# Optimization experiments

Measured on AMD Instinct MI355X. Metric: run time of the kernel, lower is better.

Reference implementation:

```python
import jax, jax.numpy as jnp
import numpy as np
import math

N, E = 100000, 1600000
IN_FEATS, H, Z_DIM, D, B_COEF = 128, 128, 32, 2, 0.2


def calc_thetas(d):
    # Bernstein-basis thetas, ascending coefficients (matches calculate_theta2)
    thetas = []
    for i in range(d + 1):
        p1 = np.zeros(i + 1); p1[i] = 0.5 ** i               # (x/2)^i
        p2 = np.array([math.comb(d - i, j) * (-0.5) ** j for j in range(d - i + 1)])  # (1-x/2)^(d-i)
        coeffs = np.convolve(p1, p2)                          # length d+1, ascending
        beta = math.gamma(i + 1) * math.gamma(d + 1 - i) / math.gamma(d + 2)
        thetas.append((coeffs / beta).tolist())
    return thetas

THETAS = calc_thetas(D)


def linear(x, w, b):
    return x @ w.T + b


def polyconv(theta, feat, src, dst, d_invsqrt, n):
    h = theta[0] * feat
    for k in range(1, len(theta)):
        tmp = feat * d_invsqrt                                # [N, F]
        agg = jax.ops.segment_sum(tmp[src], dst, num_segments=n)
        feat = feat - agg * d_invsqrt                         # (I - D^-1/2 A D^-1/2) feat
        h = h + theta[k] * feat
    return h


def enc_dec(x, w1, b1, w2, b2, src, dst, d_invsqrt, n):
    x = jax.nn.relu(linear(x, w1, b1))
    hs = jnp.concatenate([polyconv(t, x, src, dst, d_invsqrt, n) for t in THETAS], axis=-1)
    return linear(hs, w2, b2)


def setup_inputs() -> dict:
    key = jax.random.key(0)
    ks = jax.random.split(key, 16)
    nb = len(THETAS)
    return {
        "features": jax.random.normal(ks[0], (N, IN_FEATS), jnp.float32),
        "src": jax.random.randint(ks[1], (E,), 0, N, jnp.int32),
        "dst": jax.random.randint(ks[2], (E,), 0, N, jnp.int32),
        "enc_w1": jax.random.normal(ks[3], (H, IN_FEATS), jnp.float32) * 0.05,
        "enc_b1": jnp.zeros((H,), jnp.float32),
        "enc_w2": jax.random.normal(ks[4], (H, H * nb), jnp.float32) * 0.05,
        "enc_b2": jnp.zeros((H,), jnp.float32),
        "dec_w1": jax.random.normal(ks[5], (IN_FEATS, H), jnp.float32) * 0.05,
        "dec_b1": jnp.zeros((IN_FEATS,), jnp.float32),
        "dec_w2": jax.random.normal(ks[6], (IN_FEATS, IN_FEATS * nb), jnp.float32) * 0.05,
        "dec_b2": jnp.zeros((IN_FEATS,), jnp.float32),
        "rep_w": jax.random.normal(ks[7], (Z_DIM, H), jnp.float32) * 0.05,
        "rep_b": jnp.zeros((Z_DIM,), jnp.float32),
        "rec_w": jax.random.normal(ks[8], (H, Z_DIM), jnp.float32) * 0.05,
        "rec_b": jnp.zeros((H,), jnp.float32),
        "disc_w": jax.random.uniform(ks[9], (H, H), jnp.float32, -1.0 / math.sqrt(H), 1.0 / math.sqrt(H)),
    }


def reference(features, src, dst, enc_w1, enc_b1, enc_w2, enc_b2,
              dec_w1, dec_b1, dec_w2, dec_b2, rep_w, rep_b, rec_w, rec_b, disc_w):
    n = features.shape[0]
    degs = jax.ops.segment_sum(jnp.ones((src.shape[0],), jnp.float32), dst, num_segments=n)
    d_invsqrt = jnp.maximum(degs, 1.0) ** -0.5
    d_invsqrt = d_invsqrt[:, None]

    positive = enc_dec(features, enc_w1, enc_b1, enc_w2, enc_b2, src, dst, d_invsqrt, n)
    perm = jax.random.permutation(jax.random.key(7), n)
    negative = enc_dec(features[perm], enc_w1, enc_b1, enc_w2, enc_b2, src, dst, d_invsqrt, n)

    summary = jax.nn.sigmoid(positive.mean(axis=0))           # [H]
    pos_dis = positive @ (disc_w @ summary)                   # [N]
    neg_dis = negative @ (disc_w @ summary)
    # BCEWithLogits: target=1 -> softplus(-x); target=0 -> softplus(x)
    dgi_loss = jnp.mean(jax.nn.softplus(-pos_dis)) + jnp.mean(jax.nn.softplus(neg_dis))

    mu = linear(positive, rep_w, rep_b)
    log_var = mu
    eps = jax.random.normal(jax.random.key(11), mu.shape, mu.dtype)
    z = mu + eps * jnp.exp(log_var / 2)

    x_rec = enc_dec(linear(z, rec_w, rec_b), dec_w1, dec_b1, dec_w2, dec_b2, src, dst, d_invsqrt, n)
    reconst_loss = jnp.sum((x_rec - features) ** 2)
    kl_div = -0.5 * jnp.sum(1 + log_var - mu ** 2 - jnp.exp(log_var))
    vgae_loss = reconst_loss + kl_div

    ratio = jax.lax.stop_gradient(dgi_loss / vgae_loss)
    return B_COEF * dgi_loss / ratio + (1 - B_COEF) * vgae_loss
```

## Files before the change

kernel.cpp:

```cpp
#include <hip/hip_runtime.h>
#include <math.h>

#define NN   100000
#define EE   1600000
#define F    128
#define ZD   32
#define SCAN_B 256
#define PREP_BLOCKS 161
#define FC1_BLOCKS  1563
#define ENC_BLOCKS  1563
#define NBUCK 391
#define PART_CHUNK 2048
#define PART_BLOCKS 782


typedef float f32x4 __attribute__((ext_vector_type(4)));
typedef int   i32x4 __attribute__((ext_vector_type(4)));
typedef __bf16 bf16x8 __attribute__((ext_vector_type(8)));

__device__ __forceinline__ f32x4 mfma16(i32x4 a, i32x4 b, f32x4 c) {
    return __builtin_amdgcn_mfma_f32_16x16x32_bf16(
        __builtin_bit_cast(bf16x8, a), __builtin_bit_cast(bf16x8, b), c, 0, 0, 0);
}

__device__ __forceinline__ unsigned f2bf(float f) {
    unsigned u = __float_as_uint(f);
    return (u + 0x7fffu + ((u >> 16) & 1u)) >> 16;
}
__device__ __forceinline__ float bf2f(unsigned h) { return __uint_as_float(h << 16); }

__device__ __forceinline__ unsigned pcg_hash(unsigned v) {
    v = v * 747796405u + 2891336453u;
    unsigned w = ((v >> ((v >> 28u) + 4u)) ^ v) * 277803737u;
    return (w >> 22u) ^ w;
}

__device__ __forceinline__ float block_reduce_sum(float v) {
    #pragma unroll
    for (int o = 32; o > 0; o >>= 1) v += __shfl_down(v, o, 64);
    __shared__ float s[8];
    int lane = threadIdx.x & 63, w = threadIdx.x >> 6;
    if (lane == 0) s[w] = v;
    __syncthreads();
    float t = 0.f;
    if (threadIdx.x == 0) {
        int nw = (blockDim.x + 63) >> 6;
        for (int i = 0; i < nw; ++i) t += s[i];
    }
    return t;
}

__global__ __launch_bounds__(256) void prep_deg_kernel(
        const float* __restrict__ repw, const float* __restrict__ w2e,
        const float* __restrict__ b2e,  const float* __restrict__ repb,
        const float* __restrict__ w2d,
        const float* __restrict__ w1d,  const float* __restrict__ recw,
        const float* __restrict__ recb, const float* __restrict__ b1d,
        const float* __restrict__ w1e,
        unsigned short* __restrict__ Wcat,
        float* __restrict__ bmu,
        unsigned short* __restrict__ wd2_a,
        unsigned short* __restrict__ wd2_b,
        unsigned short* __restrict__ wd2_c,
        unsigned short* __restrict__ wrd,
        float* __restrict__ brd,
        unsigned short* __restrict__ w1bf,
        const int* __restrict__ dst, int* __restrict__ degs, int e) {
    int bid = blockIdx.x, tid = threadIdx.x;
    if (bid >= PREP_BLOCKS) {
        int i = (bid - PREP_BLOCKS) * 256 + tid;
        if (i < e) atomicAdd(&degs[dst[i]], 1);
        return;
    }
    if (bid < 16) {
        int idx = bid * 256 + tid;
        int i = idx >> 7, k = idx & 127;
        float m0 = 0.f, m1 = 0.f, m2 = 0.f;
        for (int h = 0; h < 128; ++h) {
            float r = repw[i * 128 + h];
            const float* wr = w2e + (size_t)h * 384 + k;
            m0 += r * wr[0];
            m1 += r * wr[128];
            m2 += r * wr[256];
        }
        Wcat[(size_t)i * 128 + k]        = (unsigned short)f2bf(3.f * m0);
        Wcat[(size_t)(32 + i) * 128 + k] = (unsigned short)f2bf(3.f * (m1 - m0));
        Wcat[(size_t)(64 + i) * 128 + k] = (unsigned short)f2bf(0.75f * m0 - 1.5f * m1 + 0.75f * m2);
    } else if (bid == 16) {
        if (tid < 32) {
            float s = repb[tid];
            for (int h = 0; h < 128; ++h) s += repw[tid * 128 + h] * b2e[h];
            bmu[tid] = s;
        }
    } else if (bid < 81) {
        int idx = (bid - 17) * 256 + tid;
        int j = idx >> 7, k = idx & 127;
        const float* wr = w2d + (size_t)j * 384 + k;
        float w0 = wr[0], w1 = wr[128], w2v = wr[256];
        wd2_a[idx] = (unsigned short)f2bf(3.f * w0);
        wd2_b[idx] = (unsigned short)f2bf(3.f * (w1 - w0));
        wd2_c[idx] = (unsigned short)f2bf(0.75f * w0 - 1.5f * w1 + 0.75f * w2v);
    } else if (bid < 97) {
        int idx = (bid - 81) * 256 + tid;
        int j = idx >> 5, i = idx & 31;
        float s = 0.f;
        for (int h = 0; h < 128; ++h) s += w1d[j * 128 + h] * recw[h * 32 + i];
        wrd[idx] = (unsigned short)f2bf(s);
        if (idx < 128) {
            float b = b1d[idx];
            for (int h = 0; h < 128; ++h) b += w1d[idx * 128 + h] * recb[h];
            brd[idx] = b;
        }
    } else {
        int idx = (bid - 97) * 256 + tid;
        w1bf[idx] = (unsigned short)f2bf(w1e[idx]);
    }
}

__global__ __launch_bounds__(SCAN_B) void scan_block_kernel(const int* __restrict__ degs,
                                                            int* __restrict__ rowstart,
                                                            int* __restrict__ blocksums,
                                                            float* __restrict__ dinv,
                                                            float* __restrict__ rsq, int n) {
    __shared__ int sh[SCAN_B];
    int i = blockIdx.x * SCAN_B + threadIdx.x;
    int v = (i < n) ? degs[i] : 0;
    int pd = (v + 15) & ~15;
    sh[threadIdx.x] = pd;
    __syncthreads();
    for (int o = 1; o < SCAN_B; o <<= 1) {
        int t = (threadIdx.x >= o) ? sh[threadIdx.x - o] : 0;
        __syncthreads();
        sh[threadIdx.x] += t;
        __syncthreads();
    }
    if (i < n) {
        rowstart[i] = sh[threadIdx.x] - pd;
        float d = fmaxf((float)v, 1.f);
        float s = sqrtf(d);
        rsq[i] = s;
        dinv[i] = 1.f / s;
    }
    if (threadIdx.x == SCAN_B - 1) blocksums[blockIdx.x] = sh[threadIdx.x];
}

__global__ __launch_bounds__(512) void scan_sums_kernel(int* __restrict__ blocksums, int nb) {
    __shared__ int sh[512];
    int v = (threadIdx.x < nb) ? blocksums[threadIdx.x] : 0;
    sh[threadIdx.x] = v;
    __syncthreads();
    for (int o = 1; o < 512; o <<= 1) {
        int t = (threadIdx.x >= o) ? sh[threadIdx.x - o] : 0;
        __syncthreads();
        sh[threadIdx.x] += t;
        __syncthreads();
    }
    if (threadIdx.x < nb) blocksums[threadIdx.x] = sh[threadIdx.x] - v;
}

__global__ __launch_bounds__(SCAN_B) void scan_add_kernel(int* __restrict__ rowstart,
                                                          int* __restrict__ cursor,
                                                          const int* __restrict__ blocksums,
                                                          const int* __restrict__ degs,
                                                          int* __restrict__ csr_src,
                                                          int* __restrict__ bstart,
                                                          int* __restrict__ bcursor,
                                                          int n) {
    int i = blockIdx.x * SCAN_B + threadIdx.x;
    if (i < n) {
        int v = rowstart[i] + blocksums[blockIdx.x];
        rowstart[i] = v;
        cursor[i] = v;
        int d = degs[i];
        int pd = (d + 15) & ~15;
        for (int j = d; j < pd; ++j) csr_src[v + j] = n;
        if ((i & 255) == 0) { bstart[i >> 8] = v; bcursor[i >> 8] = v; }
        if (i == n - 1) rowstart[n] = v + pd;
    }
}

__global__ __launch_bounds__(256) void fc1_part_kernel(const float* __restrict__ x,
                                                       const unsigned short* __restrict__ wbf,
                                                       const float* __restrict__ b,
                                                       unsigned short* __restrict__ out,
                                                       const int* __restrict__ src,
                                                       const int* __restrict__ dst,
                                                       int* __restrict__ bcursor,
                                                       int* __restrict__ ebuf,
                                                       int n, int e) {
    if (blockIdx.x >= FC1_BLOCKS) {
        __shared__ int hist[NBUCK], lofs[NBUCK], gbase[NBUCK];
        int pid = blockIdx.x - FC1_BLOCKS;
        int e0 = pid * PART_CHUNK;
        int e1 = min(e0 + PART_CHUNK, e);
        int tid = threadIdx.x;
        for (int bb = tid; bb < NBUCK; bb += 256) hist[bb] = 0;
        __syncthreads();
        for (int i = e0 + tid; i < e1; i += 256) atomicAdd(&hist[dst[i] >> 8], 1);
        __syncthreads();
        for (int bb = tid; bb < NBUCK; bb += 256) {
            int cct = hist[bb];
            gbase[bb] = cct ? atomicAdd(&bcursor[bb], cct) : 0;
            lofs[bb] = 0;
        }
        __syncthreads();
        for (int i = e0 + tid; i < e1; i += 256) {
            int d = dst[i];
            int bb = d >> 8;
            int pos = gbase[bb] + atomicAdd(&lofs[bb], 1);
            ebuf[pos] = (src[i] << 8) | (d & 255);
        }
        return;
    }
    int wv = threadIdx.x >> 6, lane = threadIdx.x & 63;
    int l16 = lane & 15, lhi = lane >> 4;
    int rowbase = blockIdx.x * 64 + wv * 16;
    int arow = rowbase + l16;
    f32x4 acc[8];
    #pragma unroll
    for (int jt = 0; jt < 8; ++jt) {
        float bj = b[jt * 16 + l16];
        acc[jt] = (f32x4){bj, bj, bj, bj};
    }
    #pragma unroll
    for (int kk = 0; kk < 4; ++kk) {
        int kbase = kk * 32 + lhi * 8;
        i32x4 afrag = {0, 0, 0, 0};
        if (arow < n) {
            const float* ap = x + (size_t)arow * F + kbase;
            f32x4 f0 = *reinterpret_cast<const f32x4*>(ap);
            f32x4 f1 = *reinterpret_cast<const f32x4*>(ap + 4);
            afrag.x = (int)(f2bf(f0.x) | (f2bf(f0.y) << 16));
            afrag.y = (int)(f2bf(f0.z) | (f2bf(f0.w) << 16));
            afrag.z = (int)(f2bf(f1.x) | (f2bf(f1.y) << 16));
            afrag.w = (int)(f2bf(f1.z) | (f2bf(f1.w) << 16));
        }
        #pragma unroll
        for (int jt = 0; jt < 8; ++jt) {
            i32x4 bfrag = *reinterpret_cast<const i32x4*>(wbf + (size_t)(jt * 16 + l16) * F + kbase);
            acc[jt] = mfma16(afrag, bfrag, acc[jt]);
        }
    }
    #pragma unroll
    for (int jt = 0; jt < 8; ++jt)
        #pragma unroll
        for (int r = 0; r < 4; ++r) {
            int row = rowbase + lhi * 4 + r;
            if (row < n)
                out[(size_t)row * F + jt * 16 + l16] =
                    (unsigned short)f2bf(fmaxf(acc[jt][r], 0.f));
        }
}

__global__ __launch_bounds__(256) void encproj_csr_kernel(const unsigned short* __restrict__ A,
                                                          const unsigned short* __restrict__ Wcat,
                                                          const float* __restrict__ dinv,
                                                          unsigned short* __restrict__ G0,
                                                          unsigned short* __restrict__ G1s,
                                                          unsigned short* __restrict__ G2s,
                                                          const int* __restrict__ ebuf,
                                                          const int* __restrict__ bstart,
                                                          const int* __restrict__ bend,
                                                          int* __restrict__ cursor,
                                                          int* __restrict__ csr_src,
                                                          int n) {
    if (blockIdx.x >= ENC_BLOCKS) {
        int bb = blockIdx.x - ENC_BLOCKS;
        int s0 = bstart[bb], s1 = bend[bb];
        for (int i = s0 + (int)threadIdx.x; i < s1; i += 256) {
            int p = ebuf[i];
            int d = (bb << 8) | (p & 255);
            int pos = atomicAdd(&cursor[d], 1);
            csr_src[pos] = p >> 8;
        }
        return;
    }
    int wv = threadIdx.x >> 6, lane = threadIdx.x & 63;
    int l16 = lane & 15, lhi = lane >> 4;
    int rowbase = blockIdx.x * 64 + wv * 16;
    int arow = rowbase + l16;
    float dv[4];
    #pragma unroll
    for (int r = 0; r < 4; ++r) {
        int row = rowbase + lhi * 4 + r;
        dv[r] = (row < n) ? dinv[row] : 1.f;
    }
    f32x4 acc[6];
    #pragma unroll
    for (int jt = 0; jt < 6; ++jt) acc[jt] = (f32x4){0.f, 0.f, 0.f, 0.f};
    #pragma unroll
    for (int kk = 0; kk < 4; ++kk) {
        int kbase = kk * 32 + lhi * 8;
        i32x4 afrag = {0, 0, 0, 0};
        if (arow < n)
            afrag = *reinterpret_cast<const i32x4*>(A + (size_t)arow * F + kbase);
        #pragma unroll
        for (int jt = 0; jt < 6; ++jt) {
            i32x4 bfrag = *reinterpret_cast<const i32x4*>(Wcat + (size_t)(jt * 16 + l16) * F + kbase);
            acc[jt] = mfma16(afrag, bfrag, acc[jt]);
        }
    }
    #pragma unroll
    for (int jt = 0; jt < 6; ++jt)
        #pragma unroll
        for (int r = 0; r < 4; ++r) {
            int row = rowbase + lhi * 4 + r;
            int j = jt * 16 + l16;
            if (row < n) {
                if (j < 32) {
                    G0[(size_t)row * 32 + j] = (unsigned short)f2bf(acc[jt][r]);
                } else if (j < 64) {
                    G1s[(size_t)row * 32 + (j - 32)] = (unsigned short)f2bf(acc[jt][r] * dv[r]);
                } else {
                    G2s[(size_t)row * 32 + (j - 64)] = (unsigned short)f2bf(acc[jt][r] * dv[r]);
                }
            }
        }
}

__global__ __launch_bounds__(256) void gather32_W_kernel(const unsigned short* __restrict__ G2s,
                                                         const unsigned short* __restrict__ G1s,
                                                         const int* __restrict__ csr_src,
                                                         const int* __restrict__ rowstart,
                                                         const float* __restrict__ dinv,
                                                         unsigned short* __restrict__ W, int n) {
    int g = threadIdx.x >> 4;
    int lane = threadIdx.x & 15;
    int r0 = blockIdx.x * 32 + g * 2;
    if (r0 >= n) return;
    int c = lane * 2;
    int start = rowstart[r0];
    int mid   = rowstart[r0 + 1];
    int end   = rowstart[r0 + 2];
    int pd0 = mid - start;
    int total = end - start;
    float ax0 = 0.f, ay0 = 0.f, ax1 = 0.f, ay1 = 0.f;
    for (int base = 0; base < total; base += 16) {
        int s = csr_src[start + base + lane];
        unsigned v[16];
        #pragma unroll
        for (int q = 0; q < 16; ++q) {
            int sq = __shfl(s, q, 16);
            v[q] = *reinterpret_cast<const unsigned*>(G2s + (size_t)sq * 32 + c);
        }
        #pragma unroll
        for (int q = 0; q < 16; ++q) {
            float vx = bf2f(v[q] & 0xffffu), vy = bf2f(v[q] >> 16);
            if (base + q < pd0) { ax0 += vx; ay0 += vy; }
            else                { ax1 += vx; ay1 += vy; }
        }
    }
    {
        float di = dinv[r0], di2 = di * di;
        unsigned g2v = *reinterpret_cast<const unsigned*>(G2s + (size_t)r0 * 32 + c);
        unsigned g1v = *reinterpret_cast<const unsigned*>(G1s + (size_t)r0 * 32 + c);
        float wx = bf2f(g1v & 0xffffu) + bf2f(g2v & 0xffffu) - di2 * ax0;
        float wy = bf2f(g1v >> 16)     + bf2f(g2v >> 16)     - di2 * ay0;
        *reinterpret_cast<unsigned*>(W + (size_t)r0 * 32 + c) = f2bf(wx) | (f2bf(wy) << 16);
    }
    if (r0 + 1 < n) {
        int r1 = r0 + 1;
        float di = dinv[r1], di2 = di * di;
        unsigned g2v = *reinterpret_cast<const unsigned*>(G2s + (size_t)r1 * 32 + c);
        unsigned g1v = *reinterpret_cast<const unsigned*>(G1s + (size_t)r1 * 32 + c);
        float wx = bf2f(g1v & 0xffffu) + bf2f(g2v & 0xffffu) - di2 * ax1;
        float wy = bf2f(g1v >> 16)     + bf2f(g2v >> 16)     - di2 * ay1;
        *reinterpret_cast<unsigned*>(W + (size_t)r1 * 32 + c) = f2bf(wx) | (f2bf(wy) << 16);
    }
}

__global__ __launch_bounds__(256) void gather32_mukl_kernel(const unsigned short* __restrict__ W,
                                                            const unsigned short* __restrict__ G0,
                                                            const int* __restrict__ csr_src,
                                                            const int* __restrict__ rowstart,
                                                            const float* __restrict__ dinv,
                                                            const float* __restrict__ rsq,
                                                            const float* __restrict__ bmu,
                                                            unsigned short* __restrict__ Z,
                                                            double* __restrict__ accd, int n) {
    int g = threadIdx.x >> 4;
    int lane = threadIdx.x & 15;
    int r0 = blockIdx.x * 32 + g * 2;
    int c = lane * 2;
    float kl = 0.f;
    if (r0 < n) {
        int start = rowstart[r0];
        int mid   = rowstart[r0 + 1];
        int end   = rowstart[r0 + 2];
        int pd0 = mid - start;
        int total = end - start;
        float axs0 = 0.f, ays0 = 0.f, axs1 = 0.f, ays1 = 0.f;
        for (int base = 0; base < total; base += 16) {
            int s = csr_src[start + base + lane];
            unsigned v[16];
            #pragma unroll
            for (int q = 0; q < 16; ++q) {
                int sq = __shfl(s, q, 16);
                v[q] = *reinterpret_cast<const unsigned*>(W + (size_t)sq * 32 + c);
            }
            #pragma unroll
            for (int q = 0; q < 16; ++q) {
                float vx = bf2f(v[q] & 0xffffu), vy = bf2f(v[q] >> 16);
                if (base + q < pd0) { axs0 += vx; ays0 += vy; }
                else                { axs1 += vx; ays1 += vy; }
            }
        }
        float axs[2] = {axs0, axs1}, ays[2] = {ays0, ays1};
        #pragma unroll
        for (int rr = 0; rr < 2; ++rr) {
            int r = r0 + rr;
            if (r < n) {
                float di = dinv[r];
                float rs = rsq[r];
                unsigned wv = *reinterpret_cast<const unsigned*>(W + (size_t)r * 32 + c);
                unsigned g0v = *reinterpret_cast<const unsigned*>(G0 + (size_t)r * 32 + c);
                float mu0 = bf2f(g0v & 0xffffu) + rs * bf2f(wv & 0xffffu) - di * axs[rr] + bmu[c];
                float mu1 = bf2f(g0v >> 16)     + rs * bf2f(wv >> 16)     - di * ays[rr] + bmu[c + 1];
                kl += (1.f + mu0 - mu0 * mu0 - expf(mu0)) + (1.f + mu1 - mu1 * mu1 - expf(mu1));
                unsigned idx0 = (unsigned)(r * ZD + c);
                unsigned h1 = pcg_hash(2u * idx0 + 1u);
                unsigned h2 = pcg_hash(2u * idx0 + 2u);
                float u1 = ((float)h1 + 0.5f) * 2.3283064365386963e-10f;
                float u2 = ((float)h2 + 0.5f) * 2.3283064365386963e-10f;
                float eps0 = sqrtf(-2.f * logf(u1)) * cosf(6.283185307179586f * u2);
                unsigned idx1 = idx0 + 1u;
                unsigned h3 = pcg_hash(2u * idx1 + 1u);
                unsigned h4 = pcg_hash(2u * idx1 + 2u);
                float u3 = ((float)h3 + 0.5f) * 2.3283064365386963e-10f;
                float u4 = ((float)h4 + 0.5f) * 2.3283064365386963e-10f;
                float eps1 = sqrtf(-2.f * logf(u3)) * cosf(6.283185307179586f * u4);
                float z0 = mu0 + eps0 * expf(0.5f * mu0);
                float z1 = mu1 + eps1 * expf(0.5f * mu1);
                *reinterpret_cast<unsigned*>(Z + (size_t)r * ZD + c) = f2bf(z0) | (f2bf(z1) << 16);
            }
        }
    }
    float bs = block_reduce_sum(kl);
    if (threadIdx.x == 0) atomicAdd(&accd[1], (double)bs);
}

__global__ __launch_bounds__(256) void gather128_kernel(const unsigned short* __restrict__ x,
                                                        const int* __restrict__ csr_src,
                                                        const int* __restrict__ rowstart,
                                                        const float* __restrict__ dinv,
                                                        unsigned short* __restrict__ out, int n) {
    int r = blockIdx.x * 4 + (threadIdx.x >> 6);
    if (r >= n) return;
    int lane = threadIdx.x & 63;
    int c = lane * 2;
    int start = rowstart[r];
    int total = rowstart[r + 1] - start;
    float ax = 0.f, ay = 0.f;
    for (int base = 0; base < total; base += 16) {
        int s = csr_src[start + base + (lane & 15)];
        unsigned v[16];
        #pragma unroll
        for (int q = 0; q < 16; ++q) {
            int sq = __shfl(s, q, 16);
            v[q] = *reinterpret_cast<const unsigned*>(x + (size_t)sq * F + c);
        }
        #pragma unroll
        for (int q = 0; q < 16; ++q) {
            ax += bf2f(v[q] & 0xffffu);
            ay += bf2f(v[q] >> 16);
        }
    }
    float di = dinv[r];
    float di2 = di * di;
    unsigned xv = *reinterpret_cast<const unsigned*>(x + (size_t)r * F + c);
    float ox = bf2f(xv & 0xffffu) - di2 * ax;
    float oy = bf2f(xv >> 16) - di2 * ay;
    *reinterpret_cast<unsigned*>(out + (size_t)r * F + c) = f2bf(ox) | (f2bf(oy) << 16);
}

__global__ __launch_bounds__(256) void recdec1_mfma_kernel(const unsigned short* __restrict__ Z,
                                                           const unsigned short* __restrict__ Wrd,
                                                           const float* __restrict__ brd,
                                                           const float* __restrict__ dinv,
                                                           unsigned short* __restrict__ out, int n) {
    int wv = threadIdx.x >> 6, lane = threadIdx.x & 63;
    int l16 = lane & 15, lhi = lane >> 4;
    int rowbase = blockIdx.x * 64 + wv * 16;
    int arow = rowbase + l16;
    int kbase = lhi * 8;
    float dv[4];
    #pragma unroll
    for (int r = 0; r < 4; ++r) {
        int row = rowbase + lhi * 4 + r;
        dv[r] = (row < n) ? dinv[row] : 1.f;
    }
    i32x4 afrag = {0, 0, 0, 0};
    if (arow < n)
        afrag = *reinterpret_cast<const i32x4*>(Z + (size_t)arow * ZD + kbase);
    #pragma unroll
    for (int jt = 0; jt < 8; ++jt) {
        float bj = brd[jt * 16 + l16];
        f32x4 acc = (f32x4){bj, bj, bj, bj};
        i32x4 bfrag = *reinterpret_cast<const i32x4*>(Wrd + (size_t)(jt * 16 + l16) * ZD + kbase);
        acc = mfma16(afrag, bfrag, acc);
        #pragma unroll
        for (int r = 0; r < 4; ++r) {
            int row = rowbase + lhi * 4 + r;
            if (row < n)
                out[(size_t)row * F + jt * 16 + l16] =
                    (unsigned short)f2bf(fmaxf(acc[r], 0.f) * dv[r]);
        }
    }
}

__global__ __launch_bounds__(256) void dec2loss_mfma_kernel(const unsigned short* __restrict__ A,
                                                            const unsigned short* __restrict__ B,
                                                            const unsigned short* __restrict__ C,
                                                            const unsigned short* __restrict__ Wa,
                                                            const unsigned short* __restrict__ Wb,
                                                            const unsigned short* __restrict__ Wc,
                                                            const float* __restrict__ b2,
                                                            const float* __restrict__ rsq,
                                                            const float* __restrict__ feats,
                                                            double* __restrict__ accd, int n) {
    __shared__ __align__(16) unsigned short wsh[128 * 128];
    int tid = threadIdx.x;
    int wv = tid >> 6, lane = tid & 63;
    int l16 = lane & 15, lhi = lane >> 4;
    int rowbase = blockIdx.x * 64 + wv * 16;
    int arow = rowbase + l16;
    float fpre[8][4];
    float rsv[4];
    #pragma unroll
    for (int r = 0; r < 4; ++r) {
        int row = rowbase + lhi * 4 + r;
        rsv[r] = (row < n) ? rsq[row] : 1.f;
    }
    #pragma unroll
    for (int jt = 0; jt < 8; ++jt)
        #pragma unroll
        for (int r = 0; r < 4; ++r) {
            int row = rowbase + lhi * 4 + r;
            fpre[jt][r] = (row < n) ? feats[(size_t)row * F + jt * 16 + l16] : 0.f;
        }
    f32x4 acc[8];
    #pragma unroll
    for (int jt = 0; jt < 8; ++jt) acc[jt] = (f32x4){0.f, 0.f, 0.f, 0.f};
    const unsigned short* mats[3] = {A, B, C};
    const unsigned short* wsrc[3] = {Wa, Wb, Wc};
    #pragma unroll
    for (int s = 0; s < 3; ++s) {
        __syncthreads();
        #pragma unroll
        for (int it = 0; it < 8; ++it) {
            int idx = it * 256 + tid;
            int j = idx >> 4;
            int colb = (idx & 15) << 4;
            i32x4 v = *reinterpret_cast<const i32x4*>(wsrc[s] + (size_t)j * 128 + ((idx & 15) << 3));
            *reinterpret_cast<i32x4*>((char*)wsh + j * 256 + (colb ^ ((j & 7) << 4))) = v;
        }
        __syncthreads();
        #pragma unroll
        for (int kk = 0; kk < 4; ++kk) {
            i32x4 afrag = {0, 0, 0, 0};
            if (arow < n)
                afrag = *reinterpret_cast<const i32x4*>(mats[s] + (size_t)arow * F + kk * 32 + lhi * 8);
            #pragma unroll
            for (int jt = 0; jt < 8; ++jt) {
                int j = jt * 16 + l16;
                int colb = (kk * 64 + lhi * 16) ^ ((j & 7) << 4);
                i32x4 bfrag = *reinterpret_cast<const i32x4*>((const char*)wsh + j * 256 + colb);
                acc[jt] = mfma16(afrag, bfrag, acc[jt]);
            }
        }
    }
    float local = 0.f;
    #pragma unroll
    for (int jt = 0; jt < 8; ++jt) {
        float bj = b2[jt * 16 + l16];
        #pragma unroll
        for (int r = 0; r < 4; ++r) {
            int row = rowbase + lhi * 4 + r;
            if (row < n) {
                float d = acc[jt][r] * rsv[r] + bj - fpre[jt][r];
                local += d * d;
            }
        }
    }
    float bs = block_reduce_sum(local);
    if (threadIdx.x == 0) atomicAdd(&accd[0], (double)bs);
}

__global__ void finalize_kernel(const double* __restrict__ acc, float* __restrict__ out) {
    out[0] = (float)(acc[0] - 0.5 * acc[1]);
}

extern "C" void kernel_launch(void* const* d_in, const int* in_sizes, int n_in,
                              void* d_out, int out_size, void* d_ws, size_t ws_size,
                              hipStream_t stream) {
    const float* feats  = (const float*)d_in[0];
    const int*   src    = (const int*)d_in[1];
    const int*   dst    = (const int*)d_in[2];
    const float* enc_w1 = (const float*)d_in[3];
    const float* enc_b1 = (const float*)d_in[4];
    const float* enc_w2 = (const float*)d_in[5];
    const float* enc_b2 = (const float*)d_in[6];
    const float* dec_w1 = (const float*)d_in[7];
    const float* dec_b1 = (const float*)d_in[8];
    const float* dec_w2 = (const float*)d_in[9];
    const float* dec_b2 = (const float*)d_in[10];
    const float* rep_w  = (const float*)d_in[11];
    const float* rep_b  = (const float*)d_in[12];
    const float* rec_w  = (const float*)d_in[13];
    const float* rec_b  = (const float*)d_in[14];

    const int n = NN, e = EE;
    char* ws = (char*)d_ws;
    size_t off = 0;
    auto alloc = [&](size_t bytes) -> void* {
        void* p = ws + off;
        off += (bytes + 255) & ~(size_t)255;
        return p;
    };
    const size_t NFB = (size_t)(n + 1) * F * sizeof(unsigned short);
    const size_t N32 = (size_t)(n + 1) * 32 * sizeof(unsigned short);
    const int nScanBlocks = (n + SCAN_B - 1) / SCAN_B;
    const int csrCap = e + 15 * NN + 64;
    int*    degs    = (int*)alloc((size_t)n * sizeof(int));
    float*  dinv    = (float*)alloc((size_t)n * sizeof(float));
    float*  rsq     = (float*)alloc((size_t)n * sizeof(float));
    int*    rowst   = (int*)alloc((size_t)(n + 1) * sizeof(int));
    int*    cursor  = (int*)alloc((size_t)n * sizeof(int));
    int*    bsums   = (int*)alloc((size_t)nScanBlocks * sizeof(int));
    int*    bstart  = (int*)alloc((NBUCK + 1) * sizeof(int));
    int*    bcursor = (int*)alloc(NBUCK * sizeof(int));
    int*    ebuf    = (int*)alloc((size_t)csrCap * sizeof(int));
    int*    csr_src = (int*)alloc((size_t)csrCap * sizeof(int));
    unsigned short* Abf = (unsigned short*)alloc(NFB);
    unsigned short* Bbf = (unsigned short*)alloc(NFB);
    unsigned short* Cbf = (unsigned short*)alloc((size_t)n * F * sizeof(unsigned short));
    unsigned short* G0  = (unsigned short*)alloc(N32);
    unsigned short* G1  = (unsigned short*)alloc(N32);
    unsigned short* G2  = (unsigned short*)alloc(N32);
    unsigned short* Wg  = (unsigned short*)alloc(N32);
    unsigned short* Zbf = (unsigned short*)alloc((size_t)n * ZD * sizeof(unsigned short));
    unsigned short* Wcat  = (unsigned short*)alloc(96 * 128 * sizeof(unsigned short));
    unsigned short* w1bf  = (unsigned short*)alloc(128 * 128 * sizeof(unsigned short));
    unsigned short* wd2_a = (unsigned short*)alloc(128 * 128 * sizeof(unsigned short));
    unsigned short* wd2_b = (unsigned short*)alloc(128 * 128 * sizeof(unsigned short));
    unsigned short* wd2_c = (unsigned short*)alloc(128 * 128 * sizeof(unsigned short));
    unsigned short* wrd   = (unsigned short*)alloc(128 * 32 * sizeof(unsigned short));
    float* bmu = (float*)alloc(32 * sizeof(float));
    float* brd = (float*)alloc(128 * sizeof(float));
    double* acc = (double*)alloc(2 * sizeof(double));

    const int gemm64   = (n + 63) / 64;
    const int csrBlks  = (e + 255) / 256;
    const int gathBlks = (n + 3) / 4;
    const int g32Blks  = (n + 31) / 32;

    hipMemsetAsync(degs, 0, (size_t)n * sizeof(int), stream);
    hipMemsetAsync(acc, 0, 2 * sizeof(double), stream);
    hipMemsetAsync(Abf + (size_t)n * F, 0, F * sizeof(unsigned short), stream);
    hipMemsetAsync(Bbf + (size_t)n * F, 0, F * sizeof(unsigned short), stream);
    hipMemsetAsync(G2 + (size_t)n * 32, 0, 32 * sizeof(unsigned short), stream);
    hipMemsetAsync(Wg + (size_t)n * 32, 0, 32 * sizeof(unsigned short), stream);

    prep_deg_kernel<<<PREP_BLOCKS + csrBlks, 256, 0, stream>>>(
        rep_w, enc_w2, enc_b2, rep_b, dec_w2, dec_w1, rec_w, rec_b, dec_b1, enc_w1,
        Wcat, bmu, wd2_a, wd2_b, wd2_c, wrd, brd, w1bf, dst, degs, e);

    scan_block_kernel<<<nScanBlocks, SCAN_B, 0, stream>>>(degs, rowst, bsums, dinv, rsq, n);
    scan_sums_kernel<<<1, 512, 0, stream>>>(bsums, nScanBlocks);
    scan_add_kernel<<<nScanBlocks, SCAN_B, 0, stream>>>(rowst, cursor, bsums, degs,
                                                        csr_src, bstart, bcursor, n);

    fc1_part_kernel<<<FC1_BLOCKS + PART_BLOCKS, 256, 0, stream>>>(
        feats, w1bf, enc_b1, Abf, src, dst, bcursor, ebuf, n, e);

    encproj_csr_kernel<<<ENC_BLOCKS + NBUCK, 256, 0, stream>>>(
        Abf, Wcat, dinv, G0, G1, G2, ebuf, bstart, bcursor, cursor, csr_src, n);

    gather32_W_kernel<<<g32Blks, 256, 0, stream>>>(G2, G1, csr_src, rowst, dinv, Wg, n);
    gather32_mukl_kernel<<<g32Blks, 256, 0, stream>>>(Wg, G0, csr_src, rowst, dinv,
                                                      rsq, bmu, Zbf, acc, n);

    recdec1_mfma_kernel<<<gemm64, 256, 0, stream>>>(Zbf, wrd, brd, dinv, Abf, n);
    gather128_kernel<<<gathBlks, 256, 0, stream>>>(Abf, csr_src, rowst, dinv, Bbf, n);
    gather128_kernel<<<gathBlks, 256, 0, stream>>>(Bbf, csr_src, rowst, dinv, Cbf, n);
    dec2loss_mfma_kernel<<<gemm64, 256, 0, stream>>>(Abf, Bbf, Cbf, wd2_a, wd2_b, wd2_c,
                                                     dec_b2, rsq, feats, acc, n);

    finalize_kernel<<<1, 1, 0, stream>>>(acc, (float*)d_out);
}
```

Before: 457.2 us.

## Compute degrees from bucketed edge buffer instead of global per-edge atomics

Replaces the per-edge global atomicAdd degree count with a per-block shared-memory histogram over 256-node buckets, plus a small scan over bucket counts. The edge partition into buckets now runs before the degree scan. Degrees are then computed per bucket with shared-memory atomics over the bucketed edge buffer. This removes 1.6M scattered global atomics, at the cost of two extra small kernel launches and an extra pass over the edge buffer.

```diff
diff --git a/kernel.cpp b/kernel.cpp
--- a/kernel.cpp
+++ b/kernel.cpp
@@ -50,7 +50,7 @@
     return t;
 }
 
-__global__ __launch_bounds__(256) void prep_deg_kernel(
+__global__ __launch_bounds__(256) void prep_bcnt_kernel(
         const float* __restrict__ repw, const float* __restrict__ w2e,
         const float* __restrict__ b2e,  const float* __restrict__ repb,
         const float* __restrict__ w2d,
@@ -65,11 +65,19 @@
         unsigned short* __restrict__ wrd,
         float* __restrict__ brd,
         unsigned short* __restrict__ w1bf,
-        const int* __restrict__ dst, int* __restrict__ degs, int e) {
+        const int* __restrict__ dst, int* __restrict__ bcnt, int e) {
     int bid = blockIdx.x, tid = threadIdx.x;
     if (bid >= PREP_BLOCKS) {
-        int i = (bid - PREP_BLOCKS) * 256 + tid;
-        if (i < e) atomicAdd(&degs[dst[i]], 1);
+        __shared__ int hist[NBUCK];
+        int pid = bid - PREP_BLOCKS;
+        int e0 = pid * PART_CHUNK;
+        int e1 = min(e0 + PART_CHUNK, e);
+        for (int bb = tid; bb < NBUCK; bb += 256) hist[bb] = 0;
+        __syncthreads();
+        for (int i = e0 + tid; i < e1; i += 256) atomicAdd(&hist[dst[i] >> 8], 1);
+        __syncthreads();
+        for (int bb = tid; bb < NBUCK; bb += 256)
+            if (hist[bb]) atomicAdd(&bcnt[bb], hist[bb]);
         return;
     }
     if (bid < 16) {
@@ -117,6 +125,43 @@
     }
 }
 
+__global__ __launch_bounds__(512) void bscan_kernel(const int* __restrict__ bcnt,
+                                                    int* __restrict__ bstart2,
+                                                    int* __restrict__ bcursor2, int e) {
+    __shared__ int sh[512];
+    int tid = threadIdx.x;
+    int v = (tid < NBUCK) ? bcnt[tid] : 0;
+    sh[tid] = v;
+    __syncthreads();
+    for (int o = 1; o < 512; o <<= 1) {
+        int t = (tid >= o) ? sh[tid - o] : 0;
+        __syncthreads();
+        sh[tid] += t;
+        __syncthreads();
+    }
+    if (tid < NBUCK) {
+        int s = sh[tid] - v;
+        bstart2[tid] = s;
+        bcursor2[tid] = s;
+    }
+    if (tid == 0) bstart2[NBUCK] = e;
+}
+
+__global__ __launch_bounds__(256) void degcnt_kernel(const int* __restrict__ ebuf,
+                                                     const int* __restrict__ bstart2,
+                                                     int* __restrict__ degs, int n) {
+    __shared__ int cnt[256];
+    int tid = threadIdx.x;
+    int bb = blockIdx.x;
+    cnt[tid] = 0;
+    __syncthreads();
+    int s0 = bstart2[bb], s1 = bstart2[bb + 1];
+    for (int i = s0 + tid; i < s1; i += 256) atomicAdd(&cnt[ebuf[i] & 255], 1);
+    __syncthreads();
+    int node = bb * 256 + tid;
+    if (node < n) degs[node] = cnt[tid];
+}
+
 __global__ __launch_bounds__(SCAN_B) void scan_block_kernel(const int* __restrict__ degs,
                                                             int* __restrict__ rowstart,
                                                             int* __restrict__ blocksums,
@@ -163,8 +208,6 @@
                                                           const int* __restrict__ blocksums,
                                                           const int* __restrict__ degs,
                                                           int* __restrict__ csr_src,
-                                                          int* __restrict__ bstart,
-                                                          int* __restrict__ bcursor,
                                                           int n) {
     int i = blockIdx.x * SCAN_B + threadIdx.x;
     if (i < n) {
@@ -174,7 +217,6 @@
         int d = degs[i];
         int pd = (d + 15) & ~15;
         for (int j = d; j < pd; ++j) csr_src[v + j] = n;
-        if ((i & 255) == 0) { bstart[i >> 8] = v; bcursor[i >> 8] = v; }
         if (i == n - 1) rowstart[n] = v + pd;
     }
 }
@@ -185,7 +227,7 @@
                                                        unsigned short* __restrict__ out,
                                                        const int* __restrict__ src,
                                                        const int* __restrict__ dst,
-                                                       int* __restrict__ bcursor,
+                                                       int* __restrict__ bcursor2,
                                                        int* __restrict__ ebuf,
                                                        int n, int e) {
     if (blockIdx.x >= FC1_BLOCKS) {
@@ -200,7 +242,7 @@
         __syncthreads();
         for (int bb = tid; bb < NBUCK; bb += 256) {
             int cct = hist[bb];
-            gbase[bb] = cct ? atomicAdd(&bcursor[bb], cct) : 0;
+            gbase[bb] = cct ? atomicAdd(&bcursor2[bb], cct) : 0;
             lofs[bb] = 0;
         }
         __syncthreads();
@@ -259,14 +301,13 @@
                                                           unsigned short* __restrict__ G1s,
                                                           unsigned short* __restrict__ G2s,
                                                           const int* __restrict__ ebuf,
-                                                          const int* __restrict__ bstart,
-                                                          const int* __restrict__ bend,
+                                                          const int* __restrict__ bstart2,
                                                           int* __restrict__ cursor,
                                                           int* __restrict__ csr_src,
                                                           int n) {
     if (blockIdx.x >= ENC_BLOCKS) {
         int bb = blockIdx.x - ENC_BLOCKS;
-        int s0 = bstart[bb], s1 = bend[bb];
+        int s0 = bstart2[bb], s1 = bstart2[bb + 1];
         for (int i = s0 + (int)threadIdx.x; i < s1; i += 256) {
             int p = ebuf[i];
             int d = (bb << 8) | (p & 255);
@@ -627,9 +668,10 @@
     int*    rowst   = (int*)alloc((size_t)(n + 1) * sizeof(int));
     int*    cursor  = (int*)alloc((size_t)n * sizeof(int));
     int*    bsums   = (int*)alloc((size_t)nScanBlocks * sizeof(int));
-    int*    bstart  = (int*)alloc((NBUCK + 1) * sizeof(int));
-    int*    bcursor = (int*)alloc(NBUCK * sizeof(int));
-    int*    ebuf    = (int*)alloc((size_t)csrCap * sizeof(int));
+    int*    bcnt    = (int*)alloc(NBUCK * sizeof(int));
+    int*    bstart2 = (int*)alloc((NBUCK + 1) * sizeof(int));
+    int*    bcursor2= (int*)alloc(NBUCK * sizeof(int));
+    int*    ebuf    = (int*)alloc((size_t)e * sizeof(int));
     int*    csr_src = (int*)alloc((size_t)csrCap * sizeof(int));
     unsigned short* Abf = (unsigned short*)alloc(NFB);
     unsigned short* Bbf = (unsigned short*)alloc(NFB);
@@ -650,31 +692,34 @@
     double* acc = (double*)alloc(2 * sizeof(double));
 
     const int gemm64   = (n + 63) / 64;
-    const int csrBlks  = (e + 255) / 256;
     const int gathBlks = (n + 3) / 4;
     const int g32Blks  = (n + 31) / 32;
 
-    hipMemsetAsync(degs, 0, (size_t)n * sizeof(int), stream);
+    hipMemsetAsync(bcnt, 0, NBUCK * sizeof(int), stream);
     hipMemsetAsync(acc, 0, 2 * sizeof(double), stream);
     hipMemsetAsync(Abf + (size_t)n * F, 0, F * sizeof(unsigned short), stream);
     hipMemsetAsync(Bbf + (size_t)n * F, 0, F * sizeof(unsigned short), stream);
     hipMemsetAsync(G2 + (size_t)n * 32, 0, 32 * sizeof(unsigned short), stream);
     hipMemsetAsync(Wg + (size_t)n * 32, 0, 32 * sizeof(unsigned short), stream);
 
-    prep_deg_kernel<<<PREP_BLOCKS + csrBlks, 256, 0, stream>>>(
+    prep_bcnt_kernel<<<PREP_BLOCKS + PART_BLOCKS, 256, 0, stream>>>(
         rep_w, enc_w2, enc_b2, rep_b, dec_w2, dec_w1, rec_w, rec_b, dec_b1, enc_w1,
-        Wcat, bmu, wd2_a, wd2_b, wd2_c, wrd, brd, w1bf, dst, degs, e);
+        Wcat, bmu, wd2_a, wd2_b, wd2_c, wrd, brd, w1bf, dst, bcnt, e);
+
+    bscan_kernel<<<1, 512, 0, stream>>>(bcnt, bstart2, bcursor2, e);
+
+    fc1_part_kernel<<<FC1_BLOCKS + PART_BLOCKS, 256, 0, stream>>>(
+        feats, w1bf, enc_b1, Abf, src, dst, bcursor2, ebuf, n, e);
+
+    degcnt_kernel<<<NBUCK, 256, 0, stream>>>(ebuf, bstart2, degs, n);
 
     scan_block_kernel<<<nScanBlocks, SCAN_B, 0, stream>>>(degs, rowst, bsums, dinv, rsq, n);
     scan_sums_kernel<<<1, 512, 0, stream>>>(bsums, nScanBlocks);
     scan_add_kernel<<<nScanBlocks, SCAN_B, 0, stream>>>(rowst, cursor, bsums, degs,
-                                                        csr_src, bstart, bcursor, n);
-
-    fc1_part_kernel<<<FC1_BLOCKS + PART_BLOCKS, 256, 0, stream>>>(
-        feats, w1bf, enc_b1, Abf, src, dst, bcursor, ebuf, n, e);
+                                                        csr_src, n);
 
     encproj_csr_kernel<<<ENC_BLOCKS + NBUCK, 256, 0, stream>>>(
-        Abf, Wcat, dinv, G0, G1, G2, ebuf, bstart, bcursor, cursor, csr_src, n);
+        Abf, Wcat, dinv, G0, G1, G2, ebuf, bstart2, cursor, csr_src, n);
 
     gather32_W_kernel<<<g32Blks, 256, 0, stream>>>(G2, G1, csr_src, rowst, dinv, Wg, n);
     gather32_mukl_kernel<<<g32Blks, 256, 0, stream>>>(Wg, G0, csr_src, rowst, dinv,
```

Measured after the change: 423.0 us. 7.5% less time.
